# Optimization experiments

Measured on AMD Instinct MI355X. Metric: run time of the kernel, lower is better.

The kernel has to match this reference:

```python
import jax, jax.numpy as jnp
import numpy as np

N = 4_194_304
DT = 1800.0   # dt_s (30-minute steps)
G = 0.76      # solar transmittance g
AZ = 41.3     # glazed area Az


def setup_inputs() -> dict:
    key = jax.random.key(0)
    ks = jax.random.split(key, 16)
    f32 = jnp.float32
    def pos(k, lo, hi):  # positive scalar param
        return jax.random.uniform(k, (), dtype=f32, minval=lo, maxval=hi)
    return {
        # RC parameters (physically positive)
        "R_ie": pos(ks[0], 0.5, 2.0),
        "R_ea": pos(ks[1], 0.5, 2.0),
        "C_in": pos(ks[2], 1e6, 5e6),
        "C_en": pos(ks[3], 1e7, 5e7),
        "a_sol_in": pos(ks[4], 0.1, 0.9),
        "a_sol_en": pos(ks[5], 0.1, 0.9),
        "a_int_in": pos(ks[6], 0.1, 0.9),
        "a_int_en": pos(ks[7], 0.1, 0.9),
        "Tin0": jax.random.uniform(ks[8], (), dtype=f32, minval=18.0, maxval=22.0),
        # driver time series
        "To": jax.random.normal(ks[9], (N,), dtype=f32) * 5.0 + 10.0,
        "Irr": jax.random.uniform(ks[10], (N,), dtype=f32, maxval=800.0),
        "Qint": jax.random.uniform(ks[11], (N,), dtype=f32, maxval=500.0),
        "Qah": jax.random.uniform(ks[12], (N,), dtype=f32, maxval=3000.0),
        "Ria": jax.random.uniform(ks[13], (N,), dtype=f32, minval=0.05, maxval=0.5),
    }


def _simulate(R_ie, R_ea, C_in, C_en, a_sol_in, a_sol_en, a_int_in, a_int_en,
              Tin0, To, Irr, Qint, Qah, Ria):
    dt = jnp.float32(DT)
    Ria_c = jnp.maximum(Ria, 1e-6)                      # (n,)
    # A matrix entries (A22 varies per step via Ria)
    A11 = -(1.0 / R_ea + 1.0 / R_ie) / C_en             # scalar
    A12 = (1.0 / R_ie) / C_en                           # scalar
    A21 = (1.0 / R_ie) / C_in                           # scalar
    A22 = -(1.0 / Ria_c + 1.0 / R_ie) / C_in            # (n,)
    # M = I - dt*A, closed-form 2x2 inverse via determinant
    M11 = 1.0 - dt * A11                                # scalar
    M12 = -dt * A12                                     # scalar
    M21 = -dt * A21                                     # scalar
    M22 = 1.0 - dt * A22                                # (n,)
    det = M11 * M22 - M12 * M21                         # (n,)
    # dt * B @ u, vectorized over all steps
    Qsol = (G * AZ) * Irr                               # (n,)
    bu0 = dt * (To / (C_en * R_ea) + (a_sol_en / C_en) * Qsol + (a_int_en / C_en) * Qint)
    bu1 = dt * (To / (C_in * Ria_c) + (a_sol_in / C_in) * Qsol + (a_int_in / C_in) * Qint + Qah / C_in)

    def step(x, inp):
        b0, b1, m22, d = inp
        r0 = x[0] + b0
        r1 = x[1] + b1
        xn0 = (m22 * r0 - M12 * r1) / d
        xn1 = (-M21 * r0 + M11 * r1) / d
        return jnp.stack([xn0, xn1]), xn1

    x0 = jnp.stack([Tin0, Tin0])
    _, Tin_seq = jax.lax.scan(step, x0, (bu0, bu1, M22, det))
    return Tin_seq                                      # (n,) indoor temps


def reference(R_ie, R_ea, C_in, C_en, a_sol_in, a_sol_en, a_int_in, a_int_en,
              Tin0, To, Irr, Qint, Qah, Ria):
    return _simulate(R_ie, R_ea, C_in, C_en, a_sol_in, a_sol_en, a_int_in, a_int_en,
                     Tin0, To, Irr, Qint, Qah, Ria)
```

## Files before the change

kernel.cpp:

```cpp
#include <hip/hip_runtime.h>

#define BLOCK 256
#define SPAN  4096

struct Xf { float p, q, r, s, u, v; };

__device__ __forceinline__ Xf xf_id() {
    Xf t; t.p = 1.f; t.q = 0.f; t.r = 0.f; t.s = 1.f; t.u = 0.f; t.v = 0.f;
    return t;
}

__device__ __forceinline__ Xf xf_compose(const Xf& E, const Xf& L) {
    Xf o;
    o.p = L.p * E.p + L.q * E.r;
    o.q = L.p * E.q + L.q * E.s;
    o.r = L.r * E.p + L.s * E.r;
    o.s = L.r * E.q + L.s * E.s;
    o.u = L.p * E.u + L.q * E.v + L.u;
    o.v = L.r * E.u + L.s * E.v + L.v;
    return o;
}

struct Par {
    float M11, M12, M21, Kx;
    float c0, c1;
    float cTo0, cIrr0, cQi0;
    float cIrr1, cQi1;
};

__device__ __forceinline__ Par make_par(
    const float* pRie, const float* pRea, const float* pCin, const float* pCen,
    const float* pAsi, const float* pAse, const float* pAii, const float* pAie)
{
    const float dt = 1800.0f;
    const float GA = 0.76f * 41.3f;
    float R_ie = *pRie, R_ea = *pRea, C_in = *pCin, C_en = *pCen;
    float asi = *pAsi, ase = *pAse, aii = *pAii, aie = *pAie;
    Par P;
    float iRie = 1.0f / R_ie;
    P.M11 = 1.0f + dt * (1.0f / R_ea + iRie) / C_en;
    P.M12 = -(dt * iRie) / C_en;
    P.M21 = -(dt * iRie) / C_in;
    P.Kx  = P.M12 * P.M21;
    P.c1  = dt / C_in;
    P.c0  = 1.0f + P.c1 * iRie;
    P.cTo0  = dt / (C_en * R_ea);
    P.cIrr0 = dt * ase * GA / C_en;
    P.cQi0  = dt * aie / C_en;
    P.cIrr1 = dt * asi * GA / C_in;
    P.cQi1  = dt * aii / C_in;
    return P;
}

__device__ __forceinline__ void storeA(float* A, int s, const Xf& v) {
    float* b = A + 6 * s + (s >> 2);
    b[0] = v.p; b[1] = v.q; b[2] = v.r; b[3] = v.s; b[4] = v.u; b[5] = v.v;
}
__device__ __forceinline__ Xf loadA(const float* A, int s) {
    const float* b = A + 6 * s + (s >> 2);
    Xf v; v.p = b[0]; v.q = b[1]; v.r = b[2]; v.s = b[3]; v.u = b[4]; v.v = b[5];
    return v;
}

__device__ __forceinline__ void sm_store(float* sm, int i, const Xf& v) {
    float* b = sm + i * 7;
    b[0] = v.p; b[1] = v.q; b[2] = v.r; b[3] = v.s; b[4] = v.u; b[5] = v.v;
}
__device__ __forceinline__ Xf sm_load(const float* sm, int i) {
    const float* b = sm + i * 7;
    Xf v; v.p = b[0]; v.q = b[1]; v.r = b[2]; v.s = b[3]; v.u = b[4]; v.v = b[5];
    return v;
}

__device__ __forceinline__ Xf block_scan(Xf v, float* sm) {
    const int t = threadIdx.x;
    sm_store(sm, t, v);
    __syncthreads();
    for (int off = 1; off < BLOCK; off <<= 1) {
        Xf e;
        bool has = (t >= off);
        if (has) e = sm_load(sm, t - off);
        __syncthreads();
        if (has) { v = xf_compose(e, v); sm_store(sm, t, v); }
        __syncthreads();
    }
    return v;
}

__global__ __launch_bounds__(BLOCK, 4) void k_blocksum(
    const float* __restrict__ To, const float* __restrict__ Irr,
    const float* __restrict__ Qi, const float* __restrict__ Qa,
    const float* __restrict__ Ra,
    const float* pRie, const float* pRea, const float* pCin, const float* pCen,
    const float* pAsi, const float* pAse, const float* pAii, const float* pAie,
    Xf* __restrict__ blkX, int N)
{
    __shared__ float smA[6400];
    __shared__ float smScan[BLOCK * 7];
    const int t = threadIdx.x;
    const int blockBase = blockIdx.x * SPAN;
    Par P = make_par(pRie, pRea, pCin, pCen, pAsi, pAse, pAii, pAie);

#pragma unroll
    for (int k = 0; k < 4; ++k) {
        const int s = t + BLOCK * k;
        const int gstep = blockBase + s * 4;
        float tox[4], irx[4], qix[4], qax[4], rax[4];
        if (gstep + 4 <= N) {
            float4 v;
            v = *(const float4*)(To  + gstep); tox[0]=v.x; tox[1]=v.y; tox[2]=v.z; tox[3]=v.w;
            v = *(const float4*)(Irr + gstep); irx[0]=v.x; irx[1]=v.y; irx[2]=v.z; irx[3]=v.w;
            v = *(const float4*)(Qi  + gstep); qix[0]=v.x; qix[1]=v.y; qix[2]=v.z; qix[3]=v.w;
            v = *(const float4*)(Qa  + gstep); qax[0]=v.x; qax[1]=v.y; qax[2]=v.z; qax[3]=v.w;
            v = *(const float4*)(Ra  + gstep); rax[0]=v.x; rax[1]=v.y; rax[2]=v.z; rax[3]=v.w;
        } else {
#pragma unroll
            for (int j = 0; j < 4; ++j) {
                int gi = gstep + j; bool val = gi < N;
                tox[j] = val ? To[gi]  : 0.f;
                irx[j] = val ? Irr[gi] : 0.f;
                qix[j] = val ? Qi[gi]  : 0.f;
                qax[j] = val ? Qa[gi]  : 0.f;
                rax[j] = val ? Ra[gi]  : 1.f;
            }
        }
        Xf sub = xf_id();
#pragma unroll
        for (int j = 0; j < 4; ++j) {
            if (gstep + j < N) {
                float rR  = __builtin_amdgcn_rcpf(fmaxf(rax[j], 1e-6f));
                float b0  = P.cTo0 * tox[j] + P.cIrr0 * irx[j] + P.cQi0 * qix[j];
                float b1  = P.c1 * fmaf(tox[j], rR, qax[j]) + P.cIrr1 * irx[j] + P.cQi1 * qix[j];
                float M22 = fmaf(P.c1, rR, P.c0);
                float det = fmaf(P.M11, M22, -P.Kx);
                float rd  = __builtin_amdgcn_rcpf(det);
                Xf T;
                T.p =  M22 * rd;
                T.q = -P.M12 * rd;
                T.r = -P.M21 * rd;
                T.s =  P.M11 * rd;
                T.u = T.p * b0 + T.q * b1;
                T.v = T.r * b0 + T.s * b1;
                sub = xf_compose(sub, T);
            }
        }
        storeA(smA, s, sub);
    }
    __syncthreads();

    Xf w = xf_id();
#pragma unroll
    for (int j = 0; j < 4; ++j) w = xf_compose(w, loadA(smA, 4 * t + j));
    Xf incl = block_scan(w, smScan);
    if (t == BLOCK - 1) blkX[blockIdx.x] = incl;
}

__global__ __launch_bounds__(BLOCK) void k_mid(
    const Xf* __restrict__ blkX, float2* __restrict__ blkSt,
    const float* pTin0, int NB)
{
    const int t = threadIdx.x;
    const int ser = (NB + BLOCK - 1) / BLOCK;
    const int base = t * ser;
    Xf acc = xf_id();
    for (int j = 0; j < ser; ++j) {
        int i = base + j;
        if (i < NB) acc = xf_compose(acc, blkX[i]);
    }
    __shared__ float sm[BLOCK * 7];
    block_scan(acc, sm);
    Xf E = xf_id();
    if (t > 0) E = sm_load(sm, t - 1);
    float T0 = *pTin0;
    float x0 = (E.p + E.q) * T0 + E.u;
    float x1 = (E.r + E.s) * T0 + E.v;
    for (int j = 0; j < ser; ++j) {
        int i = base + j;
        if (i < NB) {
            blkSt[i] = make_float2(x0, x1);
            Xf T = blkX[i];
            float n0 = T.p * x0 + T.q * x1 + T.u;
            float n1 = T.r * x0 + T.s * x1 + T.v;
            x0 = n0; x1 = n1;
        }
    }
}

__global__ __launch_bounds__(BLOCK, 4) void k_emit(
    const float* __restrict__ To, const float* __restrict__ Irr,
    const float* __restrict__ Qi, const float* __restrict__ Qa,
    const float* __restrict__ Ra,
    const float* pRie, const float* pRea, const float* pCin, const float* pCen,
    const float* pAsi, const float* pAse, const float* pAii, const float* pAie,
    const float2* __restrict__ blkSt, float* __restrict__ out, int N)
{
    __shared__ float smA[6400];
    __shared__ float smScan[BLOCK * 7];
    const int t = threadIdx.x;
    const int b = blockIdx.x;
    const int blockBase = b * SPAN;
    Par P = make_par(pRie, pRea, pCin, pCen, pAsi, pAse, pAii, pAie);

    float rRv[4][4], b0v[4][4], b1v[4][4];

#pragma unroll
    for (int k = 0; k < 4; ++k) {
        const int s = t + BLOCK * k;
        const int gstep = blockBase + s * 4;
        float tox[4], irx[4], qix[4], qax[4], rax[4];
        if (gstep + 4 <= N) {
            float4 v;
            v = *(const float4*)(To  + gstep); tox[0]=v.x; tox[1]=v.y; tox[2]=v.z; tox[3]=v.w;
            v = *(const float4*)(Irr + gstep); irx[0]=v.x; irx[1]=v.y; irx[2]=v.z; irx[3]=v.w;
            v = *(const float4*)(Qi  + gstep); qix[0]=v.x; qix[1]=v.y; qix[2]=v.z; qix[3]=v.w;
            v = *(const float4*)(Qa  + gstep); qax[0]=v.x; qax[1]=v.y; qax[2]=v.z; qax[3]=v.w;
            v = *(const float4*)(Ra  + gstep); rax[0]=v.x; rax[1]=v.y; rax[2]=v.z; rax[3]=v.w;
        } else {
#pragma unroll
            for (int j = 0; j < 4; ++j) {
                int gi = gstep + j; bool val = gi < N;
                tox[j] = val ? To[gi]  : 0.f;
                irx[j] = val ? Irr[gi] : 0.f;
                qix[j] = val ? Qi[gi]  : 0.f;
                qax[j] = val ? Qa[gi]  : 0.f;
                rax[j] = val ? Ra[gi]  : 1.f;
            }
        }
        Xf sub = xf_id();
#pragma unroll
        for (int j = 0; j < 4; ++j) {
            float rR = __builtin_amdgcn_rcpf(fmaxf(rax[j], 1e-6f));
            float b0 = P.cTo0 * tox[j] + P.cIrr0 * irx[j] + P.cQi0 * qix[j];
            float b1 = P.c1 * fmaf(tox[j], rR, qax[j]) + P.cIrr1 * irx[j] + P.cQi1 * qix[j];
            rRv[k][j] = rR; b0v[k][j] = b0; b1v[k][j] = b1;
            if (gstep + j < N) {
                float M22 = fmaf(P.c1, rR, P.c0);
                float det = fmaf(P.M11, M22, -P.Kx);
                float rd  = __builtin_amdgcn_rcpf(det);
                Xf T;
                T.p =  M22 * rd;
                T.q = -P.M12 * rd;
                T.r = -P.M21 * rd;
                T.s =  P.M11 * rd;
                T.u = T.p * b0 + T.q * b1;
                T.v = T.r * b0 + T.s * b1;
                sub = xf_compose(sub, T);
            }
        }
        storeA(smA, s, sub);
    }
    __syncthreads();

    Xf w = xf_id();
#pragma unroll
    for (int j = 0; j < 4; ++j) w = xf_compose(w, loadA(smA, 4 * t + j));
    block_scan(w, smScan);
    Xf E = (t > 0) ? sm_load(smScan, t - 1) : xf_id();

    float2 B = blkSt[b];
    float sx0 = E.p * B.x + E.q * B.y + E.u;
    float sx1 = E.r * B.x + E.s * B.y + E.v;
    float st0[4], st1[4];
#pragma unroll
    for (int j = 0; j < 4; ++j) {
        st0[j] = sx0; st1[j] = sx1;
        Xf S = loadA(smA, 4 * t + j);
        float n0 = S.p * sx0 + S.q * sx1 + S.u;
        float n1 = S.r * sx0 + S.s * sx1 + S.v;
        sx0 = n0; sx1 = n1;
    }
    __syncthreads();
#pragma unroll
    for (int j = 0; j < 4; ++j) {
        int s = 4 * t + j;
        float* pS = smA + 2 * s + (s >> 3);
        pS[0] = st0[j]; pS[1] = st1[j];
    }
    __syncthreads();

#pragma unroll
    for (int k = 0; k < 4; ++k) {
        const int s = t + BLOCK * k;
        const float* pS = smA + 2 * s + (s >> 3);
        float x0 = pS[0], x1 = pS[1];
        const int gstep = blockBase + s * 4;
        float ov[4];
#pragma unroll
        for (int j = 0; j < 4; ++j) {
            float rR  = rRv[k][j];
            float M22 = fmaf(P.c1, rR, P.c0);
            float det = fmaf(P.M11, M22, -P.Kx);
            float rd  = __builtin_amdgcn_rcpf(det);
            float r0 = x0 + b0v[k][j];
            float r1 = x1 + b1v[k][j];
            float n0 = (M22 * r0 - P.M12 * r1) * rd;
            float n1 = (P.M11 * r1 - P.M21 * r0) * rd;
            x0 = n0; x1 = n1; ov[j] = n1;
        }
        if (gstep + 4 <= N) {
            float4 o; o.x = ov[0]; o.y = ov[1]; o.z = ov[2]; o.w = ov[3];
            *(float4*)(out + gstep) = o;
        } else {
#pragma unroll
            for (int j = 0; j < 4; ++j) { int gi = gstep + j; if (gi < N) out[gi] = ov[j]; }
        }
    }
}

extern "C" void kernel_launch(void* const* d_in, const int* in_sizes, int n_in,
                              void* d_out, int out_size, void* d_ws, size_t ws_size,
                              hipStream_t stream)
{
    (void)n_in; (void)out_size; (void)ws_size;
    const float* pRie = (const float*)d_in[0];
    const float* pRea = (const float*)d_in[1];
    const float* pCin = (const float*)d_in[2];
    const float* pCen = (const float*)d_in[3];
    const float* pAsi = (const float*)d_in[4];
    const float* pAse = (const float*)d_in[5];
    const float* pAii = (const float*)d_in[6];
    const float* pAie = (const float*)d_in[7];
    const float* pTin0 = (const float*)d_in[8];
    const float* To  = (const float*)d_in[9];
    const float* Irr = (const float*)d_in[10];
    const float* Qi  = (const float*)d_in[11];
    const float* Qa  = (const float*)d_in[12];
    const float* Ra  = (const float*)d_in[13];
    float* outp = (float*)d_out;
    int N = in_sizes[9];
    if (N <= 0) return;

    const int NB = (N + SPAN - 1) / SPAN;

    Xf* blkX = (Xf*)d_ws;
    size_t off = ((size_t)NB * sizeof(Xf) + 255) & ~(size_t)255;
    float2* blkSt = (float2*)((char*)d_ws + off);

    k_blocksum<<<NB, BLOCK, 0, stream>>>(To, Irr, Qi, Qa, Ra,
        pRie, pRea, pCin, pCen, pAsi, pAse, pAii, pAie, blkX, N);
    k_mid<<<1, BLOCK, 0, stream>>>(blkX, blkSt, pTin0, NB);
    k_emit<<<NB, BLOCK, 0, stream>>>(To, Irr, Qi, Qa, Ra,
        pRie, pRea, pCin, pCen, pAsi, pAse, pAii, pAie, blkSt, outp, N);
}
```

Before: 47.43 us.

## Fuse three-pass block scan into single-pass scan with flag-based inter-block lookback

Replaces the blocksum / mid / emit three-kernel affine-transform scan with one kernel. Each block publishes its aggregate with a release flag, then waits until all earlier blocks have published and composes their aggregates with a wave-level scan. Inputs are read once instead of twice and two launches are dropped. Each block now covers 8192 steps, which raises register and LDS use per block. The scheme relies on every block being co-resident; an occupancy check chooses between it and the old three-kernel path. The look-back is O(b) per block, so the last blocks read all preceding aggregates.

```diff
diff --git a/kernel.cpp b/kernel.cpp
--- a/kernel.cpp
+++ b/kernel.cpp
@@ -1,7 +1,9 @@
 #include <hip/hip_runtime.h>
 
 #define BLOCK 256
-#define SPAN  4096
+#define SPAN_LB 8192
+#define KITER 8
+#define SPAN_FB 4096
 
 struct Xf { float p, q, r, s, u, v; };
 
@@ -61,7 +63,6 @@
     Xf v; v.p = b[0]; v.q = b[1]; v.r = b[2]; v.s = b[3]; v.u = b[4]; v.v = b[5];
     return v;
 }
-
 __device__ __forceinline__ void sm_store(float* sm, int i, const Xf& v) {
     float* b = sm + i * 7;
     b[0] = v.p; b[1] = v.q; b[2] = v.r; b[3] = v.s; b[4] = v.u; b[5] = v.v;
@@ -85,6 +86,203 @@
         __syncthreads();
     }
     return v;
+}
+
+__global__ void k_flaginit(unsigned int* __restrict__ flags, int NB) {
+    int i = blockIdx.x * blockDim.x + threadIdx.x;
+    if (i < NB) flags[i] = 0u;
+}
+
+__global__ __launch_bounds__(BLOCK, 2) void k_scan(
+    const float* __restrict__ To, const float* __restrict__ Irr,
+    const float* __restrict__ Qi, const float* __restrict__ Qa,
+    const float* __restrict__ Ra,
+    const float* pRie, const float* pRea, const float* pCin, const float* pCen,
+    const float* pAsi, const float* pAse, const float* pAii, const float* pAie,
+    const float* pTin0,
+    unsigned int* __restrict__ flags, float* __restrict__ aggs,
+    float* __restrict__ out, int N)
+{
+    __shared__ float smA[12800];
+    __shared__ float smScan[BLOCK * 7];
+    __shared__ float smE[6];
+    const int t = threadIdx.x;
+    const int b = blockIdx.x;
+    const int blockBase = b * SPAN_LB;
+    Par P = make_par(pRie, pRea, pCin, pCen, pAsi, pAse, pAii, pAie);
+
+    float rRv[KITER][4], b0v[KITER][4], b1v[KITER][4];
+
+#pragma unroll
+    for (int k = 0; k < KITER; ++k) {
+        const int s = t + BLOCK * k;
+        const int gstep = blockBase + s * 4;
+        float tox[4], irx[4], qix[4], qax[4], rax[4];
+        if (gstep + 4 <= N) {
+            float4 v;
+            v = *(const float4*)(To  + gstep); tox[0]=v.x; tox[1]=v.y; tox[2]=v.z; tox[3]=v.w;
+            v = *(const float4*)(Irr + gstep); irx[0]=v.x; irx[1]=v.y; irx[2]=v.z; irx[3]=v.w;
+            v = *(const float4*)(Qi  + gstep); qix[0]=v.x; qix[1]=v.y; qix[2]=v.z; qix[3]=v.w;
+            v = *(const float4*)(Qa  + gstep); qax[0]=v.x; qax[1]=v.y; qax[2]=v.z; qax[3]=v.w;
+            v = *(const float4*)(Ra  + gstep); rax[0]=v.x; rax[1]=v.y; rax[2]=v.z; rax[3]=v.w;
+        } else {
+#pragma unroll
+            for (int j = 0; j < 4; ++j) {
+                int gi = gstep + j; bool val = gi < N;
+                tox[j] = val ? To[gi]  : 0.f;
+                irx[j] = val ? Irr[gi] : 0.f;
+                qix[j] = val ? Qi[gi]  : 0.f;
+                qax[j] = val ? Qa[gi]  : 0.f;
+                rax[j] = val ? Ra[gi]  : 1.f;
+            }
+        }
+        Xf sub = xf_id();
+#pragma unroll
+        for (int j = 0; j < 4; ++j) {
+            float rR = __builtin_amdgcn_rcpf(fmaxf(rax[j], 1e-6f));
+            float b0 = P.cTo0 * tox[j] + P.cIrr0 * irx[j] + P.cQi0 * qix[j];
+            float b1 = P.c1 * fmaf(tox[j], rR, qax[j]) + P.cIrr1 * irx[j] + P.cQi1 * qix[j];
+            rRv[k][j] = rR; b0v[k][j] = b0; b1v[k][j] = b1;
+            if (gstep + j < N) {
+                float M22 = fmaf(P.c1, rR, P.c0);
+                float det = fmaf(P.M11, M22, -P.Kx);
+                float rd  = __builtin_amdgcn_rcpf(det);
+                Xf T;
+                T.p =  M22 * rd;
+                T.q = -P.M12 * rd;
+                T.r = -P.M21 * rd;
+                T.s =  P.M11 * rd;
+                T.u = T.p * b0 + T.q * b1;
+                T.v = T.r * b0 + T.s * b1;
+                sub = xf_compose(sub, T);
+            }
+        }
+        storeA(smA, s, sub);
+    }
+    __syncthreads();
+
+    Xf w = xf_id();
+#pragma unroll
+    for (int j = 0; j < KITER; ++j) w = xf_compose(w, loadA(smA, KITER * t + j));
+    Xf incl = block_scan(w, smScan);
+    Xf E = (t > 0) ? sm_load(smScan, t - 1) : xf_id();
+
+    if (t == BLOCK - 1) {
+        float* dst = aggs + 6 * b;
+        __hip_atomic_store(dst + 0, incl.p, __ATOMIC_RELAXED, __HIP_MEMORY_SCOPE_AGENT);
+        __hip_atomic_store(dst + 1, incl.q, __ATOMIC_RELAXED, __HIP_MEMORY_SCOPE_AGENT);
+        __hip_atomic_store(dst + 2, incl.r, __ATOMIC_RELAXED, __HIP_MEMORY_SCOPE_AGENT);
+        __hip_atomic_store(dst + 3, incl.s, __ATOMIC_RELAXED, __HIP_MEMORY_SCOPE_AGENT);
+        __hip_atomic_store(dst + 4, incl.u, __ATOMIC_RELAXED, __HIP_MEMORY_SCOPE_AGENT);
+        __hip_atomic_store(dst + 5, incl.v, __ATOMIC_RELAXED, __HIP_MEMORY_SCOPE_AGENT);
+        __hip_atomic_store(&flags[b], 1u, __ATOMIC_RELEASE, __HIP_MEMORY_SCOPE_AGENT);
+    }
+
+    if (b == 0) {
+        if (t == 0) {
+            smE[0] = 1.f; smE[1] = 0.f; smE[2] = 0.f;
+            smE[3] = 1.f; smE[4] = 0.f; smE[5] = 0.f;
+        }
+    } else if (t < 64) {
+        for (;;) {
+            bool myready = true;
+            for (int i = t; i < b; i += 64)
+                if (__hip_atomic_load(&flags[i], __ATOMIC_ACQUIRE, __HIP_MEMORY_SCOPE_AGENT) == 0u)
+                    myready = false;
+            if (__all(myready)) break;
+            __builtin_amdgcn_s_sleep(2);
+        }
+        Xf acc = xf_id();
+        for (int base = 0; base < b; base += 64) {
+            int idx = base + t;
+            Xf v = xf_id();
+            if (idx < b) {
+                const float* src = aggs + 6 * idx;
+                v.p = __hip_atomic_load(src + 0, __ATOMIC_RELAXED, __HIP_MEMORY_SCOPE_AGENT);
+                v.q = __hip_atomic_load(src + 1, __ATOMIC_RELAXED, __HIP_MEMORY_SCOPE_AGENT);
+                v.r = __hip_atomic_load(src + 2, __ATOMIC_RELAXED, __HIP_MEMORY_SCOPE_AGENT);
+                v.s = __hip_atomic_load(src + 3, __ATOMIC_RELAXED, __HIP_MEMORY_SCOPE_AGENT);
+                v.u = __hip_atomic_load(src + 4, __ATOMIC_RELAXED, __HIP_MEMORY_SCOPE_AGENT);
+                v.v = __hip_atomic_load(src + 5, __ATOMIC_RELAXED, __HIP_MEMORY_SCOPE_AGENT);
+            }
+#pragma unroll
+            for (int sft = 1; sft < 64; sft <<= 1) {
+                Xf u;
+                u.p = __shfl_up(v.p, sft, 64);
+                u.q = __shfl_up(v.q, sft, 64);
+                u.r = __shfl_up(v.r, sft, 64);
+                u.s = __shfl_up(v.s, sft, 64);
+                u.u = __shfl_up(v.u, sft, 64);
+                u.v = __shfl_up(v.v, sft, 64);
+                if (t >= sft) v = xf_compose(u, v);
+            }
+            Xf wacc;
+            wacc.p = __shfl(v.p, 63, 64);
+            wacc.q = __shfl(v.q, 63, 64);
+            wacc.r = __shfl(v.r, 63, 64);
+            wacc.s = __shfl(v.s, 63, 64);
+            wacc.u = __shfl(v.u, 63, 64);
+            wacc.v = __shfl(v.v, 63, 64);
+            acc = xf_compose(acc, wacc);
+        }
+        if (t == 0) {
+            smE[0] = acc.p; smE[1] = acc.q; smE[2] = acc.r;
+            smE[3] = acc.s; smE[4] = acc.u; smE[5] = acc.v;
+        }
+    }
+    __syncthreads();
+
+    float T0 = *pTin0;
+    float xb0 = (smE[0] + smE[1]) * T0 + smE[4];
+    float xb1 = (smE[2] + smE[3]) * T0 + smE[5];
+
+    float sx0 = E.p * xb0 + E.q * xb1 + E.u;
+    float sx1 = E.r * xb0 + E.s * xb1 + E.v;
+    float st0[KITER], st1[KITER];
+#pragma unroll
+    for (int j = 0; j < KITER; ++j) {
+        st0[j] = sx0; st1[j] = sx1;
+        Xf S = loadA(smA, KITER * t + j);
+        float n0 = S.p * sx0 + S.q * sx1 + S.u;
+        float n1 = S.r * sx0 + S.s * sx1 + S.v;
+        sx0 = n0; sx1 = n1;
+    }
+    __syncthreads();
+#pragma unroll
+    for (int j = 0; j < KITER; ++j) {
+        int s = KITER * t + j;
+        float* pS = smA + 2 * s + (s >> 3);
+        pS[0] = st0[j]; pS[1] = st1[j];
+    }
+    __syncthreads();
+
+#pragma unroll
+    for (int k = 0; k < KITER; ++k) {
+        const int s = t + BLOCK * k;
+        const float* pS = smA + 2 * s + (s >> 3);
+        float x0 = pS[0], x1 = pS[1];
+        const int gstep = blockBase + s * 4;
+        float ov[4];
+#pragma unroll
+        for (int j = 0; j < 4; ++j) {
+            float rR  = rRv[k][j];
+            float M22 = fmaf(P.c1, rR, P.c0);
+            float det = fmaf(P.M11, M22, -P.Kx);
+            float rd  = __builtin_amdgcn_rcpf(det);
+            float r0 = x0 + b0v[k][j];
+            float r1 = x1 + b1v[k][j];
+            float n0 = (M22 * r0 - P.M12 * r1) * rd;
+            float n1 = (P.M11 * r1 - P.M21 * r0) * rd;
+            x0 = n0; x1 = n1; ov[j] = n1;
+        }
+        if (gstep + 4 <= N) {
+            float4 o; o.x = ov[0]; o.y = ov[1]; o.z = ov[2]; o.w = ov[3];
+            *(float4*)(out + gstep) = o;
+        } else {
+#pragma unroll
+            for (int j = 0; j < 4; ++j) { int gi = gstep + j; if (gi < N) out[gi] = ov[j]; }
+        }
+    }
 }
 
 __global__ __launch_bounds__(BLOCK, 4) void k_blocksum(
@@ -98,7 +296,7 @@
     __shared__ float smA[6400];
     __shared__ float smScan[BLOCK * 7];
     const int t = threadIdx.x;
-    const int blockBase = blockIdx.x * SPAN;
+    const int blockBase = blockIdx.x * SPAN_FB;
     Par P = make_par(pRie, pRea, pCin, pCen, pAsi, pAse, pAii, pAie);
 
 #pragma unroll
@@ -198,7 +396,7 @@
     __shared__ float smScan[BLOCK * 7];
     const int t = threadIdx.x;
     const int b = blockIdx.x;
-    const int blockBase = b * SPAN;
+    const int blockBase = b * SPAN_FB;
     Par P = make_par(pRie, pRea, pCin, pCen, pAsi, pAse, pAii, pAie);
 
     float rRv[4][4], b0v[4][4], b1v[4][4];
@@ -330,15 +528,33 @@
     int N = in_sizes[9];
     if (N <= 0) return;
 
-    const int NB = (N + SPAN - 1) / SPAN;
-
-    Xf* blkX = (Xf*)d_ws;
-    size_t off = ((size_t)NB * sizeof(Xf) + 255) & ~(size_t)255;
-    float2* blkSt = (float2*)((char*)d_ws + off);
-
-    k_blocksum<<<NB, BLOCK, 0, stream>>>(To, Irr, Qi, Qa, Ra,
-        pRie, pRea, pCin, pCen, pAsi, pAse, pAii, pAie, blkX, N);
-    k_mid<<<1, BLOCK, 0, stream>>>(blkX, blkSt, pTin0, NB);
-    k_emit<<<NB, BLOCK, 0, stream>>>(To, Irr, Qi, Qa, Ra,
-        pRie, pRea, pCin, pCen, pAsi, pAse, pAii, pAie, blkSt, outp, N);
-}
+    const int NB = (N + SPAN_LB - 1) / SPAN_LB;
+
+    int dev = 0;
+    hipGetDevice(&dev);
+    int numCU = 0;
+    hipDeviceGetAttribute(&numCU, hipDeviceAttributeMultiprocessorCount, dev);
+    int maxb = 0;
+    hipOccupancyMaxActiveBlocksPerMultiprocessor(&maxb, (const void*)k_scan, BLOCK, 0);
+    bool ok = (maxb > 0) && ((long long)maxb * (long long)numCU >= (long long)NB);
+
+    if (ok) {
+        unsigned int* flags = (unsigned int*)d_ws;
+        size_t off = (((size_t)NB * 4) + 255) & ~(size_t)255;
+        float* aggs = (float*)((char*)d_ws + off);
+        k_flaginit<<<(NB + BLOCK - 1) / BLOCK, BLOCK, 0, stream>>>(flags, NB);
+        k_scan<<<NB, BLOCK, 0, stream>>>(To, Irr, Qi, Qa, Ra,
+            pRie, pRea, pCin, pCen, pAsi, pAse, pAii, pAie, pTin0,
+            flags, aggs, outp, N);
+    } else {
+        const int NB3 = (N + SPAN_FB - 1) / SPAN_FB;
+        Xf* blkX = (Xf*)d_ws;
+        size_t off = ((size_t)NB3 * sizeof(Xf) + 255) & ~(size_t)255;
+        float2* blkSt = (float2*)((char*)d_ws + off);
+        k_blocksum<<<NB3, BLOCK, 0, stream>>>(To, Irr, Qi, Qa, Ra,
+            pRie, pRea, pCin, pCen, pAsi, pAse, pAii, pAie, blkX, N);
+        k_mid<<<1, BLOCK, 0, stream>>>(blkX, blkSt, pTin0, NB3);
+        k_emit<<<NB3, BLOCK, 0, stream>>>(To, Irr, Qi, Qa, Ra,
+            pRie, pRea, pCin, pCen, pAsi, pAse, pAii, pAie, blkSt, outp, N);
+    }
+}
```

Result: no change. 47.32 us (-0.2%).

## Replace shared-memory block scans with wavefront shuffle scans and smaller spans

Applied to the files above, without the earlier changes.

Both block-level kernels now do the affine-transform scan with 64-lane wavefront shuffles instead of a log-step shared-memory scan with many barriers. Each block covers a span half the previous size, processed in two chunks of 1024 steps, with per-wave aggregates combined through a tiny shared buffer. Launch bounds for the reduce kernel are raised to allow more resident blocks. The aim is to cut barrier count and shared-memory traffic. In exchange there are twice as many blocks and a longer serial mid-level scan.

```diff
diff --git a/kernel.cpp b/kernel.cpp
--- a/kernel.cpp
+++ b/kernel.cpp
@@ -1,7 +1,8 @@
 #include <hip/hip_runtime.h>
 
 #define BLOCK 256
-#define SPAN  4096
+#define SPAN  2048
+#define ITERS 2
 
 struct Xf { float p, q, r, s, u, v; };
 
@@ -52,14 +53,126 @@
     return P;
 }
 
-__device__ __forceinline__ void storeA(float* A, int s, const Xf& v) {
-    float* b = A + 6 * s + (s >> 2);
+__device__ __forceinline__ Xf step_xf(const Par& P, float to, float ir, float qi,
+                                      float qa, float ra,
+                                      float* rRo, float* b0o, float* b1o)
+{
+    float rR  = __builtin_amdgcn_rcpf(fmaxf(ra, 1e-6f));
+    float b0  = P.cTo0 * to + P.cIrr0 * ir + P.cQi0 * qi;
+    float b1  = P.c1 * fmaf(to, rR, qa) + P.cIrr1 * ir + P.cQi1 * qi;
+    float M22 = fmaf(P.c1, rR, P.c0);
+    float det = fmaf(P.M11, M22, -P.Kx);
+    float rd  = __builtin_amdgcn_rcpf(det);
+    Xf T;
+    T.p =  M22 * rd;
+    T.q = -P.M12 * rd;
+    T.r = -P.M21 * rd;
+    T.s =  P.M11 * rd;
+    T.u = T.p * b0 + T.q * b1;
+    T.v = T.r * b0 + T.s * b1;
+    if (rRo) { *rRo = rR; *b0o = b0; *b1o = b1; }
+    return T;
+}
+
+__device__ __forceinline__ Xf shfl_down_xf(const Xf& v, int d) {
+    Xf o;
+    o.p = __shfl_down(v.p, d, 64);
+    o.q = __shfl_down(v.q, d, 64);
+    o.r = __shfl_down(v.r, d, 64);
+    o.s = __shfl_down(v.s, d, 64);
+    o.u = __shfl_down(v.u, d, 64);
+    o.v = __shfl_down(v.v, d, 64);
+    return o;
+}
+__device__ __forceinline__ Xf shfl_up_xf(const Xf& v, int d) {
+    Xf o;
+    o.p = __shfl_up(v.p, d, 64);
+    o.q = __shfl_up(v.q, d, 64);
+    o.r = __shfl_up(v.r, d, 64);
+    o.s = __shfl_up(v.s, d, 64);
+    o.u = __shfl_up(v.u, d, 64);
+    o.v = __shfl_up(v.v, d, 64);
+    return o;
+}
+
+__device__ __forceinline__ void sm6_store(float* b, const Xf& v) {
     b[0] = v.p; b[1] = v.q; b[2] = v.r; b[3] = v.s; b[4] = v.u; b[5] = v.v;
 }
-__device__ __forceinline__ Xf loadA(const float* A, int s) {
-    const float* b = A + 6 * s + (s >> 2);
+__device__ __forceinline__ Xf sm6_load(const float* b) {
     Xf v; v.p = b[0]; v.q = b[1]; v.r = b[2]; v.s = b[3]; v.u = b[4]; v.v = b[5];
     return v;
+}
+
+__device__ __forceinline__ void load4(
+    const float* __restrict__ To, const float* __restrict__ Irr,
+    const float* __restrict__ Qi, const float* __restrict__ Qa,
+    const float* __restrict__ Ra, int gstep, int N,
+    float* tox, float* irx, float* qix, float* qax, float* rax)
+{
+    if (gstep + 4 <= N) {
+        float4 v;
+        v = *(const float4*)(To  + gstep); tox[0]=v.x; tox[1]=v.y; tox[2]=v.z; tox[3]=v.w;
+        v = *(const float4*)(Irr + gstep); irx[0]=v.x; irx[1]=v.y; irx[2]=v.z; irx[3]=v.w;
+        v = *(const float4*)(Qi  + gstep); qix[0]=v.x; qix[1]=v.y; qix[2]=v.z; qix[3]=v.w;
+        v = *(const float4*)(Qa  + gstep); qax[0]=v.x; qax[1]=v.y; qax[2]=v.z; qax[3]=v.w;
+        v = *(const float4*)(Ra  + gstep); rax[0]=v.x; rax[1]=v.y; rax[2]=v.z; rax[3]=v.w;
+    } else {
+#pragma unroll
+        for (int j = 0; j < 4; ++j) {
+            int gi = gstep + j; bool val = gi < N;
+            tox[j] = val ? To[gi]  : 0.f;
+            irx[j] = val ? Irr[gi] : 0.f;
+            qix[j] = val ? Qi[gi]  : 0.f;
+            qax[j] = val ? Qa[gi]  : 0.f;
+            rax[j] = val ? Ra[gi]  : 1.f;
+        }
+    }
+}
+
+__global__ __launch_bounds__(BLOCK, 8) void k_blocksum(
+    const float* __restrict__ To, const float* __restrict__ Irr,
+    const float* __restrict__ Qi, const float* __restrict__ Qa,
+    const float* __restrict__ Ra,
+    const float* pRie, const float* pRea, const float* pCin, const float* pCen,
+    const float* pAsi, const float* pAse, const float* pAii, const float* pAie,
+    Xf* __restrict__ blkX, int N)
+{
+    __shared__ float smW[4 * 6];
+    const int t = threadIdx.x;
+    const int lane = t & 63;
+    const int w = t >> 6;
+    const int blockBase = blockIdx.x * SPAN;
+    Par P = make_par(pRie, pRea, pCin, pCen, pAsi, pAse, pAii, pAie);
+
+    Xf blockAgg = xf_id();
+#pragma unroll
+    for (int iter = 0; iter < ITERS; ++iter) {
+        const int gstep = blockBase + iter * 1024 + 4 * t;
+        float tox[4], irx[4], qix[4], qax[4], rax[4];
+        load4(To, Irr, Qi, Qa, Ra, gstep, N, tox, irx, qix, qax, rax);
+        Xf v = xf_id();
+#pragma unroll
+        for (int j = 0; j < 4; ++j)
+            if (gstep + j < N)
+                v = xf_compose(v, step_xf(P, tox[j], irx[j], qix[j], qax[j], rax[j],
+                                          nullptr, nullptr, nullptr));
+#pragma unroll
+        for (int d = 1; d < 64; d <<= 1) {
+            Xf u = shfl_down_xf(v, d);
+            v = xf_compose(v, u);
+        }
+        if (lane == 0) sm6_store(smW + w * 6, v);
+        __syncthreads();
+        if (t == 0) {
+            Xf ia = sm6_load(smW + 0);
+            ia = xf_compose(ia, sm6_load(smW + 6));
+            ia = xf_compose(ia, sm6_load(smW + 12));
+            ia = xf_compose(ia, sm6_load(smW + 18));
+            blockAgg = xf_compose(blockAgg, ia);
+        }
+        __syncthreads();
+    }
+    if (t == 0) blkX[blockIdx.x] = blockAgg;
 }
 
 __device__ __forceinline__ void sm_store(float* sm, int i, const Xf& v) {
@@ -71,7 +184,6 @@
     Xf v; v.p = b[0]; v.q = b[1]; v.r = b[2]; v.s = b[3]; v.u = b[4]; v.v = b[5];
     return v;
 }
-
 __device__ __forceinline__ Xf block_scan(Xf v, float* sm) {
     const int t = threadIdx.x;
     sm_store(sm, t, v);
@@ -85,74 +197,6 @@
         __syncthreads();
     }
     return v;
-}
-
-__global__ __launch_bounds__(BLOCK, 4) void k_blocksum(
-    const float* __restrict__ To, const float* __restrict__ Irr,
-    const float* __restrict__ Qi, const float* __restrict__ Qa,
-    const float* __restrict__ Ra,
-    const float* pRie, const float* pRea, const float* pCin, const float* pCen,
-    const float* pAsi, const float* pAse, const float* pAii, const float* pAie,
-    Xf* __restrict__ blkX, int N)
-{
-    __shared__ float smA[6400];
-    __shared__ float smScan[BLOCK * 7];
-    const int t = threadIdx.x;
-    const int blockBase = blockIdx.x * SPAN;
-    Par P = make_par(pRie, pRea, pCin, pCen, pAsi, pAse, pAii, pAie);
-
-#pragma unroll
-    for (int k = 0; k < 4; ++k) {
-        const int s = t + BLOCK * k;
-        const int gstep = blockBase + s * 4;
-        float tox[4], irx[4], qix[4], qax[4], rax[4];
-        if (gstep + 4 <= N) {
-            float4 v;
-            v = *(const float4*)(To  + gstep); tox[0]=v.x; tox[1]=v.y; tox[2]=v.z; tox[3]=v.w;
-            v = *(const float4*)(Irr + gstep); irx[0]=v.x; irx[1]=v.y; irx[2]=v.z; irx[3]=v.w;
-            v = *(const float4*)(Qi  + gstep); qix[0]=v.x; qix[1]=v.y; qix[2]=v.z; qix[3]=v.w;
-            v = *(const float4*)(Qa  + gstep); qax[0]=v.x; qax[1]=v.y; qax[2]=v.z; qax[3]=v.w;
-            v = *(const float4*)(Ra  + gstep); rax[0]=v.x; rax[1]=v.y; rax[2]=v.z; rax[3]=v.w;
-        } else {
-#pragma unroll
-            for (int j = 0; j < 4; ++j) {
-                int gi = gstep + j; bool val = gi < N;
-                tox[j] = val ? To[gi]  : 0.f;
-                irx[j] = val ? Irr[gi] : 0.f;
-                qix[j] = val ? Qi[gi]  : 0.f;
-                qax[j] = val ? Qa[gi]  : 0.f;
-                rax[j] = val ? Ra[gi]  : 1.f;
-            }
-        }
-        Xf sub = xf_id();
-#pragma unroll
-        for (int j = 0; j < 4; ++j) {
-            if (gstep + j < N) {
-                float rR  = __builtin_amdgcn_rcpf(fmaxf(rax[j], 1e-6f));
-                float b0  = P.cTo0 * tox[j] + P.cIrr0 * irx[j] + P.cQi0 * qix[j];
-                float b1  = P.c1 * fmaf(tox[j], rR, qax[j]) + P.cIrr1 * irx[j] + P.cQi1 * qix[j];
-                float M22 = fmaf(P.c1, rR, P.c0);
-                float det = fmaf(P.M11, M22, -P.Kx);
-                float rd  = __builtin_amdgcn_rcpf(det);
-                Xf T;
-                T.p =  M22 * rd;
-                T.q = -P.M12 * rd;
-                T.r = -P.M21 * rd;
-                T.s =  P.M11 * rd;
-                T.u = T.p * b0 + T.q * b1;
-                T.v = T.r * b0 + T.s * b1;
-                sub = xf_compose(sub, T);
-            }
-        }
-        storeA(smA, s, sub);
-    }
-    __syncthreads();
-
-    Xf w = xf_id();
-#pragma unroll
-    for (int j = 0; j < 4; ++j) w = xf_compose(w, loadA(smA, 4 * t + j));
-    Xf incl = block_scan(w, smScan);
-    if (t == BLOCK - 1) blkX[blockIdx.x] = incl;
 }
 
 __global__ __launch_bounds__(BLOCK) void k_mid(
@@ -194,105 +238,61 @@
     const float* pAsi, const float* pAse, const float* pAii, const float* pAie,
     const float2* __restrict__ blkSt, float* __restrict__ out, int N)
 {
-    __shared__ float smA[6400];
-    __shared__ float smScan[BLOCK * 7];
+    __shared__ float smW[4 * ITERS * 6];
     const int t = threadIdx.x;
-    const int b = blockIdx.x;
-    const int blockBase = b * SPAN;
+    const int lane = t & 63;
+    const int w = t >> 6;
+    const int blockBase = blockIdx.x * SPAN;
     Par P = make_par(pRie, pRea, pCin, pCen, pAsi, pAse, pAii, pAie);
 
-    float rRv[4][4], b0v[4][4], b1v[4][4];
-
-#pragma unroll
-    for (int k = 0; k < 4; ++k) {
-        const int s = t + BLOCK * k;
-        const int gstep = blockBase + s * 4;
+    float rRv[ITERS][4], b0v[ITERS][4], b1v[ITERS][4];
+    Xf sc[ITERS];
+
+#pragma unroll
+    for (int iter = 0; iter < ITERS; ++iter) {
+        const int gstep = blockBase + iter * 1024 + 4 * t;
         float tox[4], irx[4], qix[4], qax[4], rax[4];
-        if (gstep + 4 <= N) {
-            float4 v;
-            v = *(const float4*)(To  + gstep); tox[0]=v.x; tox[1]=v.y; tox[2]=v.z; tox[3]=v.w;
-            v = *(const float4*)(Irr + gstep); irx[0]=v.x; irx[1]=v.y; irx[2]=v.z; irx[3]=v.w;
-            v = *(const float4*)(Qi  + gstep); qix[0]=v.x; qix[1]=v.y; qix[2]=v.z; qix[3]=v.w;
-            v = *(const float4*)(Qa  + gstep); qax[0]=v.x; qax[1]=v.y; qax[2]=v.z; qax[3]=v.w;
-            v = *(const float4*)(Ra  + gstep); rax[0]=v.x; rax[1]=v.y; rax[2]=v.z; rax[3]=v.w;
-        } else {
-#pragma unroll
-            for (int j = 0; j < 4; ++j) {
-                int gi = gstep + j; bool val = gi < N;
-                tox[j] = val ? To[gi]  : 0.f;
-                irx[j] = val ? Irr[gi] : 0.f;
-                qix[j] = val ? Qi[gi]  : 0.f;
-                qax[j] = val ? Qa[gi]  : 0.f;
-                rax[j] = val ? Ra[gi]  : 1.f;
-            }
-        }
-        Xf sub = xf_id();
+        load4(To, Irr, Qi, Qa, Ra, gstep, N, tox, irx, qix, qax, rax);
+        Xf v = xf_id();
 #pragma unroll
         for (int j = 0; j < 4; ++j) {
-            float rR = __builtin_amdgcn_rcpf(fmaxf(rax[j], 1e-6f));
-            float b0 = P.cTo0 * tox[j] + P.cIrr0 * irx[j] + P.cQi0 * qix[j];
-            float b1 = P.c1 * fmaf(tox[j], rR, qax[j]) + P.cIrr1 * irx[j] + P.cQi1 * qix[j];
-            rRv[k][j] = rR; b0v[k][j] = b0; b1v[k][j] = b1;
-            if (gstep + j < N) {
-                float M22 = fmaf(P.c1, rR, P.c0);
-                float det = fmaf(P.M11, M22, -P.Kx);
-                float rd  = __builtin_amdgcn_rcpf(det);
-                Xf T;
-                T.p =  M22 * rd;
-                T.q = -P.M12 * rd;
-                T.r = -P.M21 * rd;
-                T.s =  P.M11 * rd;
-                T.u = T.p * b0 + T.q * b1;
-                T.v = T.r * b0 + T.s * b1;
-                sub = xf_compose(sub, T);
-            }
-        }
-        storeA(smA, s, sub);
+            Xf T = step_xf(P, tox[j], irx[j], qix[j], qax[j], rax[j],
+                           &rRv[iter][j], &b0v[iter][j], &b1v[iter][j]);
+            if (gstep + j < N) v = xf_compose(v, T);
+        }
+#pragma unroll
+        for (int d = 1; d < 64; d <<= 1) {
+            Xf u = shfl_up_xf(v, d);
+            if (lane >= d) v = xf_compose(u, v);
+        }
+        sc[iter] = v;
+        if (lane == 63) sm6_store(smW + (w * ITERS + iter) * 6, v);
     }
     __syncthreads();
 
-    Xf w = xf_id();
-#pragma unroll
-    for (int j = 0; j < 4; ++j) w = xf_compose(w, loadA(smA, 4 * t + j));
-    block_scan(w, smScan);
-    Xf E = (t > 0) ? sm_load(smScan, t - 1) : xf_id();
-
-    float2 B = blkSt[b];
-    float sx0 = E.p * B.x + E.q * B.y + E.u;
-    float sx1 = E.r * B.x + E.s * B.y + E.v;
-    float st0[4], st1[4];
-#pragma unroll
-    for (int j = 0; j < 4; ++j) {
-        st0[j] = sx0; st1[j] = sx1;
-        Xf S = loadA(smA, 4 * t + j);
-        float n0 = S.p * sx0 + S.q * sx1 + S.u;
-        float n1 = S.r * sx0 + S.s * sx1 + S.v;
-        sx0 = n0; sx1 = n1;
-    }
-    __syncthreads();
-#pragma unroll
-    for (int j = 0; j < 4; ++j) {
-        int s = 4 * t + j;
-        float* pS = smA + 2 * s + (s >> 3);
-        pS[0] = st0[j]; pS[1] = st1[j];
-    }
-    __syncthreads();
-
-#pragma unroll
-    for (int k = 0; k < 4; ++k) {
-        const int s = t + BLOCK * k;
-        const float* pS = smA + 2 * s + (s >> 3);
-        float x0 = pS[0], x1 = pS[1];
-        const int gstep = blockBase + s * 4;
+    float2 B = blkSt[blockIdx.x];
+    float Sx = B.x, Sy = B.y;
+#pragma unroll
+    for (int iter = 0; iter < ITERS; ++iter) {
+        Xf Wpre = xf_id();
+        for (int ww = 0; ww < w; ++ww)
+            Wpre = xf_compose(Wpre, sm6_load(smW + (ww * ITERS + iter) * 6));
+        Xf lex = shfl_up_xf(sc[iter], 1);
+        if (lane == 0) lex = xf_id();
+        Xf E = xf_compose(Wpre, lex);
+        float x0 = E.p * Sx + E.q * Sy + E.u;
+        float x1 = E.r * Sx + E.s * Sy + E.v;
+
+        const int gstep = blockBase + iter * 1024 + 4 * t;
         float ov[4];
 #pragma unroll
         for (int j = 0; j < 4; ++j) {
-            float rR  = rRv[k][j];
+            float rR  = rRv[iter][j];
             float M22 = fmaf(P.c1, rR, P.c0);
             float det = fmaf(P.M11, M22, -P.Kx);
             float rd  = __builtin_amdgcn_rcpf(det);
-            float r0 = x0 + b0v[k][j];
-            float r1 = x1 + b1v[k][j];
+            float r0 = x0 + b0v[iter][j];
+            float r1 = x1 + b1v[iter][j];
             float n0 = (M22 * r0 - P.M12 * r1) * rd;
             float n1 = (P.M11 * r1 - P.M21 * r0) * rd;
             x0 = n0; x1 = n1; ov[j] = n1;
@@ -304,6 +304,14 @@
 #pragma unroll
             for (int j = 0; j < 4; ++j) { int gi = gstep + j; if (gi < N) out[gi] = ov[j]; }
         }
+
+        Xf A = sm6_load(smW + (0 * ITERS + iter) * 6);
+        A = xf_compose(A, sm6_load(smW + (1 * ITERS + iter) * 6));
+        A = xf_compose(A, sm6_load(smW + (2 * ITERS + iter) * 6));
+        A = xf_compose(A, sm6_load(smW + (3 * ITERS + iter) * 6));
+        float nSx = A.p * Sx + A.q * Sy + A.u;
+        float nSy = A.r * Sx + A.s * Sy + A.v;
+        Sx = nSx; Sy = nSy;
     }
 }
 
```

After: 49.48 us. +4.3%, slower.
